# Optimization experiments

Hardware: AMD Instinct MI355X
Metric: run time of the kernel (lower is better)

The kernel has to match this reference:

```python
import jax, jax.numpy as jnp
import numpy as np

IN_MODES = (4, 4, 6, 8)  # prod = 768 = d_model; same modes for input and output
D_MODEL = 768
N_HEADS = 12
D_HEAD = D_MODEL // N_HEADS
SCALE = 1.0 / np.sqrt(D_HEAD)
TT_RANKS = (1, 32, 64, 32, 1)


def tt_linear(x, c0, c1, c2, c3, b):
    # TT-factorized linear: cores c_k have shape (r_{k-1}, m_k, n_k, r_k)
    # with in/out modes IN_MODES. x: [B, S, 768]
    B, S, D = x.shape
    t = x.reshape(B * S, *IN_MODES)                     # n i j k l over in-modes
    t = jnp.einsum('nijkl,mir->njklmr', t, c0[0])       # contract n1, r0=1 squeezed
    t = jnp.einsum('njklmr,rpjs->nklmps', t, c1)        # contract n2 and rank r1
    t = jnp.einsum('nklmps,sqkt->nlmpqt', t, c2)        # contract n3 and rank r2
    t = jnp.einsum('nlmpqt,tul->nmpqu', t, c3[..., 0])  # contract n4 and rank r3, r4=1
    return t.reshape(B, S, D) + b                        # out-modes m,p,q,u -> 768


def _make_tt_params(key):
    ks = jax.random.split(key, 4)
    cores = []
    for i in range(4):
        shape = (TT_RANKS[i], IN_MODES[i], IN_MODES[i], TT_RANKS[i + 1])
        cores.append(jax.random.normal(ks[i], shape, jnp.float32) * 0.05)
    bias = jnp.zeros((D_MODEL,), jnp.float32)
    return cores, bias


def setup_inputs() -> dict:
    key = jax.random.key(0)
    kx, kq, kk, kv, ko = jax.random.split(key, 5)
    B, S = 2, 2048
    x = jax.random.normal(kx, (B, S, D_MODEL), jnp.float32)
    mask = jnp.tril(jnp.ones((S, S), dtype=bool))[None, None]  # causal [1,1,S,S]
    out = {'x': x, 'mask': mask}
    for name, k in (('q', kq), ('k', kk), ('v', kv), ('o', ko)):
        cores, bias = _make_tt_params(k)
        for i in range(4):
            out[f'{name}c{i}'] = cores[i]
        out[f'{name}b'] = bias
    return out


def reference(x, mask,
              qc0, qc1, qc2, qc3, qb,
              kc0, kc1, kc2, kc3, kb,
              vc0, vc1, vc2, vc3, vb,
              oc0, oc1, oc2, oc3, ob):
    B, S, _ = x.shape
    q = tt_linear(x, qc0, qc1, qc2, qc3, qb)
    k = tt_linear(x, kc0, kc1, kc2, kc3, kb)
    v = tt_linear(x, vc0, vc1, vc2, vc3, vb)
    # [B, S, H, Dh] -> [B, H, S, Dh]
    q = q.reshape(B, S, N_HEADS, D_HEAD).transpose(0, 2, 1, 3)
    k = k.reshape(B, S, N_HEADS, D_HEAD).transpose(0, 2, 1, 3)
    v = v.reshape(B, S, N_HEADS, D_HEAD).transpose(0, 2, 1, 3)
    scores = jnp.einsum('bhqd,bhkd->bhqk', q, k) * SCALE  # full O(S^2) scores
    scores = jnp.where(mask, scores, jnp.float32(-10000.0))  # masked_fill(mask==0,-1e4)
    attn = jax.nn.softmax(scores, axis=-1)  # dropout is identity at eval
    out = jnp.einsum('bhqk,bhkd->bhqd', attn, v)
    out = out.transpose(0, 2, 1, 3).reshape(B, S, D_MODEL)
    return tt_linear(out, oc0, oc1, oc2, oc3, ob)
```

## Files before the change

### kernel.cpp

```cpp
#include <hip/hip_runtime.h>
#include <cstddef>
#include <cstdint>

#define D_MODEL 768
#define N_HEADS 12
#define SEQ 2048
#define BATCH 2
#define NROWS (BATCH * SEQ)
#define W_ELEMS (D_MODEL * D_MODEL)
#define Y_ELEMS (NROWS * D_MODEL)

typedef __attribute__((ext_vector_type(8))) short bf16x8;
typedef __attribute__((ext_vector_type(4))) float f32x4;

struct TTPtrs {
    const float* c0[4];
    const float* c1[4];
    const float* c2[4];
    const float* c3[4];
};

__device__ __forceinline__ float bf2f(uint16_t u) {
    union { uint32_t u; float f; } c; c.u = ((uint32_t)u) << 16; return c.f;
}
__device__ __forceinline__ uint16_t f2bf(float f) {
    union { float f; uint32_t u; } c; c.f = f;
    uint32_t x = c.u + 0x7fffu + ((c.u >> 16) & 1u);
    return (uint16_t)(x >> 16);
}
__device__ __forceinline__ uint32_t cvtpk(float lo, float hi) {
    uint32_t r;
    asm("v_cvt_pk_bf16_f32 %0, %1, %2" : "=v"(r) : "v"(lo), "v"(hi));
    return r;
}
__device__ __forceinline__ void glds16(const void* g, void* l) {
    auto gp = reinterpret_cast<const __attribute__((address_space(1))) uint32_t*>(
        reinterpret_cast<uintptr_t>(g));
    auto lp = reinterpret_cast<__attribute__((address_space(3))) uint32_t*>(
        reinterpret_cast<uintptr_t>(l));
    __builtin_amdgcn_global_load_lds(gp, lp, 16, 0, 0);
}

__global__ __launch_bounds__(256) void pre_kernel(TTPtrs P, float* __restrict__ wsA,
                                                  const float* __restrict__ x,
                                                  uint16_t* __restrict__ xb) {
    const int bx = blockIdx.x;
    if (bx < 256) {
        const int mat = bx >> 6;
        const float* c0 = P.c0[mat];
        const float* c1 = P.c1[mat];
        float* A = wsA + mat * 16384;
        int idx = (bx & 63) * 256 + threadIdx.x;
        int s = idx & 63, pj = (idx >> 6) & 15, mi = idx >> 10;
        float acc = 0.f;
        #pragma unroll 8
        for (int r = 0; r < 32; r++)
            acc = fmaf(c0[mi * 32 + r], c1[(r * 16 + pj) * 64 + s], acc);
        A[idx] = acc;
    } else {
        int idx = ((bx - 256) * 256 + threadIdx.x) * 4;
        float4 v = *(const float4*)(x + idx);
        *(uint2*)(xb + idx) = make_uint2(cvtpk(v.x, v.y), cvtpk(v.z, v.w));
    }
}

__global__ __launch_bounds__(256) void tt_buildB(TTPtrs P, const float* __restrict__ wsA,
                                                 float* __restrict__ wsB) {
    const int mat = blockIdx.y;
    const float* c2 = P.c2[mat];
    const float* A = wsA + mat * 16384;
    float* B = wsB + (size_t)mat * 294912;
    int idx = blockIdx.x * 256 + threadIdx.x;
    int t = idx & 31;
    int rest = idx >> 5;
    int qk = rest % 36;
    int rest2 = rest / 36;
    int pj = rest2 & 15, mi = rest2 >> 4;
    const float* Arow = A + (mi * 16 + pj) * 64;
    float acc = 0.f;
    #pragma unroll 8
    for (int s = 0; s < 64; s++)
        acc = fmaf(Arow[s], c2[(s * 36 + qk) * 32 + t], acc);
    B[idx] = acc;
}

__global__ __launch_bounds__(256) void tt_buildC(TTPtrs P, const float* __restrict__ wsB,
                                                 uint16_t* __restrict__ Wbf) {
    __shared__ float b_lds[36 * 33];
    __shared__ float c_lds[32 * 64];
    const int mat = blockIdx.y;
    const int mipj = blockIdx.x;
    const int mi = mipj >> 4, pj = mipj & 15;
    const int m = mi >> 2, i = mi & 3, p = pj >> 2, j = pj & 3;
    const float* Bsrc = wsB + (size_t)mat * 294912 + (size_t)mipj * 1152;
    const float* c3 = P.c3[mat];
    uint16_t* Wt = Wbf + (size_t)mat * W_ELEMS;
    const int tid = threadIdx.x;

    for (int e = tid; e < 1152; e += 256) {
        int qk = e >> 5, t = e & 31;
        b_lds[qk * 33 + t] = Bsrc[e];
    }
    for (int e = tid; e < 2048; e += 256)
        c_lds[e] = c3[e];
    __syncthreads();

    const int outbase = (m * 4 + p) * 48;
    const int inbase = (i * 4 + j) * 48;
    #pragma unroll
    for (int n = 0; n < 9; n++) {
        int idx = n * 256 + tid;
        int qu = idx / 48, kl = idx % 48;
        int q = qu >> 3, u = qu & 7, k = kl >> 3, l = kl & 7;
        const float* brow = &b_lds[(q * 6 + k) * 33];
        const float* crow = &c_lds[u * 8 + l];
        float acc = 0.f;
        #pragma unroll 8
        for (int t = 0; t < 32; t++)
            acc = fmaf(brow[t], crow[t * 64], acc);
        Wt[(size_t)(outbase + qu) * D_MODEL + inbase + kl] = f2bf(acc);
    }
}

template <int MODE>
__global__ __launch_bounds__(256) void gemm_mfma(const uint16_t* __restrict__ X,
                                                 const uint16_t* __restrict__ Wall,
                                                 const float* __restrict__ b0,
                                                 const float* __restrict__ b1,
                                                 const float* __restrict__ b2,
                                                 void* __restrict__ Yall,
                                                 uint16_t* __restrict__ Vt) {
    __shared__ uint16_t lds[2][8192];
    const int z = blockIdx.z;
    const uint16_t* W = Wall + (size_t)z * W_ELEMS;
    const float* bias = (z == 0) ? b0 : (z == 1 ? b1 : b2);
    const int m0 = blockIdx.x * 128, n0 = blockIdx.y * 128;
    const int tid = threadIdx.x, w = tid >> 6, l = tid & 63;
    const int wr = w >> 1, wc = w & 1;
    const int l15 = l & 15, lg = l >> 4;

    const int srow = w * 32 + (l >> 2);
    const int scol = ((l & 3) ^ ((l >> 2) & 3)) * 8;
    const uint16_t* Abase = X + (size_t)(m0 + srow) * D_MODEL + scol;
    const uint16_t* Bbase = W + (size_t)(n0 + srow) * D_MODEL + scol;

    f32x4 acc[4][4];
    #pragma unroll
    for (int mi = 0; mi < 4; ++mi)
        #pragma unroll
        for (int ni = 0; ni < 4; ++ni) acc[mi][ni] = (f32x4){0.f, 0.f, 0.f, 0.f};

    auto stage = [&](int buf, int kt) {
        const uint16_t* A0 = Abase + kt * 32;
        const uint16_t* B0 = Bbase + kt * 32;
        glds16(A0, &lds[buf][w * 1024]);
        glds16(A0 + 16 * D_MODEL, &lds[buf][w * 1024 + 512]);
        glds16(B0, &lds[buf][4096 + w * 1024]);
        glds16(B0 + 16 * D_MODEL, &lds[buf][4096 + w * 1024 + 512]);
    };

    stage(0, 0);
    __syncthreads();
    const int roff = ((lg ^ (l & 3)) << 3);
    for (int kt = 0; kt < 24; ++kt) {
        int cur = kt & 1;
        if (kt < 23) stage(cur ^ 1, kt + 1);
        const uint16_t* As = &lds[cur][0];
        const uint16_t* Bs = &lds[cur][4096];
        bf16x8 a[4], bb[4];
        #pragma unroll
        for (int mi = 0; mi < 4; ++mi)
            a[mi] = *(const bf16x8*)(As + (wr * 64 + mi * 16 + l15) * 32 + roff);
        #pragma unroll
        for (int ni = 0; ni < 4; ++ni)
            bb[ni] = *(const bf16x8*)(Bs + (wc * 64 + ni * 16 + l15) * 32 + roff);
        #pragma unroll
        for (int mi = 0; mi < 4; ++mi)
            #pragma unroll
            for (int ni = 0; ni < 4; ++ni)
                acc[mi][ni] = __builtin_amdgcn_mfma_f32_16x16x32_bf16(
                    a[mi], bb[ni], acc[mi][ni], 0, 0, 0);
        __syncthreads();
    }

    float bv[4];
    #pragma unroll
    for (int ni = 0; ni < 4; ++ni) bv[ni] = bias[n0 + wc * 64 + ni * 16 + l15];

    if (MODE == 1 && z == 2) {
        uint16_t* T = &lds[0][0];
        #pragma unroll
        for (int mi = 0; mi < 4; ++mi) {
            int row = wr * 64 + mi * 16 + lg * 4;
            #pragma unroll
            for (int ni = 0; ni < 4; ++ni) {
                int col = wc * 64 + ni * 16 + l15;
                float v0 = acc[mi][ni][0] + bv[ni], v1 = acc[mi][ni][1] + bv[ni];
                float v2 = acc[mi][ni][2] + bv[ni], v3 = acc[mi][ni][3] + bv[ni];
                int byte = (col << 8) + (row << 1);
                byte ^= (((col & 31) ^ (row >> 6)) << 3);
                *(uint2*)((char*)T + byte) = make_uint2(cvtpk(v0, v1), cvtpk(v2, v3));
            }
        }
        __syncthreads();
        int col = tid >> 1, half = tid & 1;
        int gcol = n0 + col;
        int bb_ = m0 >> 11;
        int s = (m0 & 2047) + half * 64;
        uint16_t* dst = Vt + ((size_t)(bb_ * 12 + (gcol >> 6)) * 64 + (gcol & 63)) * 2048 + s;
        uint2 tv[16];
        #pragma unroll
        for (int k = 0; k < 16; ++k) {
            int r = half * 64 + k * 4;
            int byte = (col << 8) + (r << 1);
            byte ^= (((col & 31) ^ (r >> 6)) << 3);
            tv[k] = *(const uint2*)((const char*)T + byte);
        }
        #pragma unroll
        for (int k = 0; k < 8; ++k)
            *(uint4*)(dst + k * 8) = make_uint4(tv[2 * k].x, tv[2 * k].y,
                                                tv[2 * k + 1].x, tv[2 * k + 1].y);
    } else {
        #pragma unroll
        for (int mi = 0; mi < 4; ++mi)
            #pragma unroll
            for (int ni = 0; ni < 4; ++ni)
                #pragma unroll
                for (int r = 0; r < 4; ++r) {
                    int row = m0 + wr * 64 + mi * 16 + lg * 4 + r;
                    int col = n0 + wc * 64 + ni * 16 + l15;
                    float v = acc[mi][ni][r] + bv[ni];
                    if (MODE == 1)
                        ((uint16_t*)Yall + (size_t)z * Y_ELEMS)[(size_t)row * D_MODEL + col] = f2bf(v);
                    else
                        ((float*)Yall)[(size_t)row * D_MODEL + col] = v;
                }
    }
}

__global__ __launch_bounds__(256) void attn_mfma(const uint16_t* __restrict__ Q,
                                                 const uint16_t* __restrict__ K,
                                                 const uint16_t* __restrict__ Vt,
                                                 uint16_t* __restrict__ pO1,
                                                 uint16_t* __restrict__ pO2,
                                                 float* __restrict__ tbuf) {
    __shared__ uint16_t ks[2][4096];
    __shared__ uint16_t vs[2][4096];
    __shared__ uint16_t ps[4][1024];

    const int bx = blockIdx.x;
    const int u = bx / 24;
    const int bh = bx % 24;
    int g, c;
    if (u < 32)      { g = u >> 2,            c = u & 3; }
    else if (u < 56) { int t = u - 32; g = 8 + t / 3,  c = t % 3; }
    else if (u < 72) { int t = u - 56; g = 16 + (t >> 1), c = t & 1; }
    else             { g = 24 + (u - 72),     c = 0; }
    const int qt = 31 - g;
    const int ktlo = c * 8;
    const int kthi = min(ktlo + 7, qt);
    const int nkt = kthi - ktlo + 1;

    const int b = bh / 12, h = bh % 12;
    const int tid = threadIdx.x, w = tid >> 6, l = tid & 63;
    const int l15 = l & 15, lg = l >> 4;
    const size_t headoff = (size_t)b * SEQ * D_MODEL + h * 64;
    const size_t vhead = ((size_t)(b * 12 + h)) << 17;
    const int sc8 = ((l & 7) ^ ((l >> 3) & 7)) * 8;
    const int srow = w * 16 + (l >> 3);

    const float QS = 0.125f * 1.44269504088896f;
    bf16x8 qf[2];
    {
        const uint16_t* qp = Q + headoff + (size_t)(qt * 64 + w * 16 + l15) * D_MODEL + lg * 8;
        #pragma unroll
        for (int ds = 0; ds < 2; ++ds) {
            bf16x8 qv = *(const bf16x8*)(qp + ds * 32);
            #pragma unroll
            for (int j = 0; j < 8; ++j)
                qf[ds][j] = (short)f2bf(bf2f((uint16_t)qv[j]) * QS);
        }
    }

    float m_ = -3e38f, l_ = 0.f;
    f32x4 oacc[4];
    #pragma unroll
    for (int ni = 0; ni < 4; ++ni) oacc[ni] = (f32x4){0.f, 0.f, 0.f, 0.f};
    const int qglob = qt * 64 + w * 16 + l15;

    auto stage = [&](int buf, int kt) {
        const uint16_t* ksrc = K + headoff + (size_t)(kt * 64 + srow) * D_MODEL + sc8;
        glds16(ksrc, &ks[buf][w * 1024]);
        glds16(ksrc + 8 * D_MODEL, &ks[buf][w * 1024 + 512]);
        const uint16_t* vsrc = Vt + vhead + (size_t)srow * SEQ + kt * 64 + sc8;
        glds16(vsrc, &vs[buf][w * 1024]);
        glds16(vsrc + 8 * SEQ, &vs[buf][w * 1024 + 512]);
    };

    stage(0, ktlo);
    for (int it = 0; it < nkt; ++it) {
        const int kt = ktlo + it;
        const int cur = it & 1;
        __syncthreads();
        if (it + 1 < nkt) stage(cur ^ 1, kt + 1);

        f32x4 sacc[4];
        #pragma unroll
        for (int ki = 0; ki < 4; ++ki) sacc[ki] = (f32x4){0.f, 0.f, 0.f, 0.f};
        __builtin_amdgcn_s_setprio(1);
        #pragma unroll
        for (int ds = 0; ds < 2; ++ds)
            #pragma unroll
            for (int ki = 0; ki < 4; ++ki) {
                int byte = (ki * 16 + l15) * 128 + ((((ds << 2) + lg) ^ (l15 & 7)) << 4);
                bf16x8 ak = *(const bf16x8*)((const char*)&ks[cur][0] + byte);
                sacc[ki] = __builtin_amdgcn_mfma_f32_16x16x32_bf16(ak, qf[ds], sacc[ki], 0, 0, 0);
            }
        __builtin_amdgcn_s_setprio(0);

        const bool diag = (kt == qt);
        float sv[16];
        #pragma unroll
        for (int ki = 0; ki < 4; ++ki)
            #pragma unroll
            for (int r = 0; r < 4; ++r) {
                float s = sacc[ki][r];
                if (diag) {
                    int key = kt * 64 + ki * 16 + lg * 4 + r;
                    if (key > qglob) s = -3e38f;
                }
                sv[ki * 4 + r] = s;
            }
        float mx = fmaxf(fmaxf(sv[0], sv[1]), sv[2]);
        #pragma unroll
        for (int i = 3; i < 15; i += 2) mx = fmaxf(fmaxf(mx, sv[i]), sv[i + 1]);
        mx = fmaxf(mx, sv[15]);
        mx = fmaxf(mx, __shfl_xor(mx, 16));
        mx = fmaxf(mx, __shfl_xor(mx, 32));
        if (__any(mx > m_ + 11.54f)) {
            float mnew = fmaxf(m_, mx);
            float alpha = __builtin_amdgcn_exp2f(m_ - mnew);
            l_ *= alpha;
            float a0 = __shfl(alpha, lg * 4 + 0), a1 = __shfl(alpha, lg * 4 + 1);
            float a2 = __shfl(alpha, lg * 4 + 2), a3 = __shfl(alpha, lg * 4 + 3);
            #pragma unroll
            for (int ni = 0; ni < 4; ++ni) {
                oacc[ni][0] *= a0; oacc[ni][1] *= a1;
                oacc[ni][2] *= a2; oacc[ni][3] *= a3;
            }
            m_ = mnew;
        }
        float sum = 0.f;
        uint32_t pk[8];
        #pragma unroll
        for (int i = 0; i < 16; i += 2) {
            float p0 = __builtin_amdgcn_exp2f(sv[i] - m_);
            float p1 = __builtin_amdgcn_exp2f(sv[i + 1] - m_);
            sum += p0 + p1;
            pk[i >> 1] = cvtpk(p0, p1);
        }
        sum += __shfl_xor(sum, 16);
        sum += __shfl_xor(sum, 32);
        l_ += sum;

        uint16_t* psw = &ps[w][0];
        #pragma unroll
        for (int ki = 0; ki < 4; ++ki) {
            int byte = (l15 * 128 + ki * 32 + lg * 8) ^ ((l15 & 7) << 4);
            *(uint2*)((char*)psw + byte) = make_uint2(pk[ki * 2], pk[ki * 2 + 1]);
        }
        asm volatile("s_waitcnt lgkmcnt(0)" ::: "memory");
        __builtin_amdgcn_sched_barrier(0);

        __builtin_amdgcn_s_setprio(1);
        #pragma unroll
        for (int kss = 0; kss < 2; ++kss) {
            int pbyte = l15 * 128 + ((((kss << 2) + lg) ^ (l15 & 7)) << 4);
            bf16x8 ap = *(const bf16x8*)((const char*)psw + pbyte);
            #pragma unroll
            for (int ni = 0; ni < 4; ++ni) {
                int vbyte = (ni * 16 + l15) * 128 + ((((kss << 2) + lg) ^ (l15 & 7)) << 4);
                bf16x8 bv = *(const bf16x8*)((const char*)&vs[cur][0] + vbyte);
                oacc[ni] = __builtin_amdgcn_mfma_f32_16x16x32_bf16(ap, bv, oacc[ni], 0, 0, 0);
            }
        }
        __builtin_amdgcn_s_setprio(0);
    }

    float li0 = 1.f / __shfl(l_, lg * 4 + 0), li1 = 1.f / __shfl(l_, lg * 4 + 1);
    float li2 = 1.f / __shfl(l_, lg * 4 + 2), li3 = 1.f / __shfl(l_, lg * 4 + 3);
    uint16_t* op = (bx < 1536) ? (pO1 + (size_t)bx * 4096)
                               : (pO2 + (size_t)(bx - 1536) * 4096);
    #pragma unroll
    for (int ni = 0; ni < 4; ++ni) {
        int col = ni * 16 + l15;
        int rbase = (w * 16 + lg * 4) * 64 + col;
        op[rbase + 0 * 64] = f2bf(oacc[ni][0] * li0);
        op[rbase + 1 * 64] = f2bf(oacc[ni][1] * li1);
        op[rbase + 2 * 64] = f2bf(oacc[ni][2] * li2);
        op[rbase + 3 * 64] = f2bf(oacc[ni][3] * li3);
    }
    if (lg == 0)
        tbuf[(size_t)bx * 64 + w * 16 + l15] = m_ + __log2f(l_);
}

__global__ __launch_bounds__(256) void attn_combine(const uint16_t* __restrict__ pO1,
                                                    const uint16_t* __restrict__ pO2,
                                                    const float* __restrict__ tbuf,
                                                    uint16_t* __restrict__ Obf) {
    __shared__ float t_lds[4][64];
    const int bx = blockIdx.x;
    const int qt = bx & 31, bh = bx >> 5;
    const int b = bh / 12, h = bh % 12;
    const int g = 31 - qt;
    const int u_base = (g < 8) ? 4 * g : (g < 16) ? 32 + 3 * (g - 8)
                     : (g < 24) ? 56 + 2 * (g - 16) : 72 + (g - 24);
    const int nc = (g < 8) ? 4 : (g < 16) ? 3 : (g < 24) ? 2 : 1;
    const int tid = threadIdx.x;
    if (tid < nc * 64) {
        int c = tid >> 6, q = tid & 63;
        t_lds[c][q] = tbuf[(size_t)((u_base + c) * 24 + bh) * 64 + q];
    }
    __syncthreads();

    const int q = tid >> 2, d0 = (tid & 3) * 16;
    float tmax = t_lds[0][q];
    for (int c = 1; c < nc; ++c) tmax = fmaxf(tmax, t_lds[c][q]);
    float acc[16];
    #pragma unroll
    for (int j = 0; j < 16; ++j) acc[j] = 0.f;
    float denom = 0.f;
    for (int c = 0; c < nc; ++c) {
        float wgt = __builtin_amdgcn_exp2f(t_lds[c][q] - tmax);
        denom += wgt;
        int ug = (u_base + c) * 24 + bh;
        const uint16_t* op = (ug < 1536) ? (pO1 + (size_t)ug * 4096)
                                         : (pO2 + (size_t)(ug - 1536) * 4096);
        bf16x8 v0 = *(const bf16x8*)(op + q * 64 + d0);
        bf16x8 v1 = *(const bf16x8*)(op + q * 64 + d0 + 8);
        #pragma unroll
        for (int j = 0; j < 8; ++j) {
            acc[j]     += bf2f((uint16_t)v0[j]) * wgt;
            acc[8 + j] += bf2f((uint16_t)v1[j]) * wgt;
        }
    }
    float inv = 1.f / denom;
    uint32_t outp[8];
    #pragma unroll
    for (int j = 0; j < 8; ++j)
        outp[j] = cvtpk(acc[2 * j] * inv, acc[2 * j + 1] * inv);
    size_t rb = (size_t)(b * SEQ + qt * 64 + q) * D_MODEL + h * 64 + d0;
    *(uint4*)(Obf + rb)     = make_uint4(outp[0], outp[1], outp[2], outp[3]);
    *(uint4*)(Obf + rb + 8) = make_uint4(outp[4], outp[5], outp[6], outp[7]);
}

extern "C" void kernel_launch(void* const* d_in, const int* in_sizes, int n_in,
                              void* d_out, int out_size, void* d_ws, size_t ws_size,
                              hipStream_t stream) {
    const float* x = (const float*)d_in[0];
    TTPtrs P;
    const float* biases[4];
    const int base[4] = {2, 7, 12, 17};
    for (int t = 0; t < 4; t++) {
        P.c0[t] = (const float*)d_in[base[t] + 0];
        P.c1[t] = (const float*)d_in[base[t] + 1];
        P.c2[t] = (const float*)d_in[base[t] + 2];
        P.c3[t] = (const float*)d_in[base[t] + 3];
        biases[t] = (const float*)d_in[base[t] + 4];
    }

    char* ws = (char*)d_ws;
    float* wsA = (float*)(ws + 0);
    float* wsB = (float*)(ws + 262144);
    uint16_t* Wbf = (uint16_t*)(ws + 4980736);
    uint16_t* xbf = (uint16_t*)(ws + 9699328);
    uint16_t* pO2 = (uint16_t*)(ws + 9699328);
    float* tbuf = (float*)(ws + 12845056);
    uint16_t* Qbf = (uint16_t*)(ws + 15990784);
    uint16_t* Kbf = (uint16_t*)(ws + 22282240);
    uint16_t* Vtbf = (uint16_t*)(ws + 28573696);
    uint16_t* Obf = (uint16_t*)(ws + 34865152);
    uint16_t* pO1 = (uint16_t*)d_out;
    (void)Kbf;

    pre_kernel<<<dim3(256 + 3072), 256, 0, stream>>>(P, wsA, x, xbf);
    tt_buildB<<<dim3(1152, 4), 256, 0, stream>>>(P, wsA, wsB);
    tt_buildC<<<dim3(256, 4), 256, 0, stream>>>(P, wsB, Wbf);

    gemm_mfma<1><<<dim3(32, 6, 3), 256, 0, stream>>>(xbf, Wbf, biases[0], biases[1],
                                                     biases[2], (void*)Qbf, Vtbf);
    attn_mfma<<<dim3(1920), 256, 0, stream>>>(Qbf, Kbf, Vtbf, pO1, pO2, tbuf);
    attn_combine<<<dim3(768), 256, 0, stream>>>(pO1, pO2, tbuf, Obf);

    gemm_mfma<0><<<dim3(32, 6, 1), 256, 0, stream>>>(Obf, Wbf + 3 * (size_t)W_ELEMS,
                                                     biases[3], biases[3], biases[3],
                                                     d_out, nullptr);
}
```

Measured before the change: 237.8 us.

## Fuse three TT weight-build kernels and x conversion into one kernel

Merges the pre_kernel (A = c0·c1), tt_buildB (B = A·c2) and tt_buildC (W = B·c3) stages into a single wbuild kernel. Each block recomputes its 64-entry A row and its 1152-entry B slice in shared memory instead of writing them to workspace and reading them back. This removes two kernel launches and the global round-trips for the intermediates. In exchange, each block reads c2 from global memory (L2-cached) and does a longer serial stage, so per-block latency grows.

```diff
diff --git a/kernel.cpp b/kernel.cpp
--- a/kernel.cpp
+++ b/kernel.cpp
@@ -41,68 +41,50 @@
     __builtin_amdgcn_global_load_lds(gp, lp, 16, 0, 0);
 }
 
-__global__ __launch_bounds__(256) void pre_kernel(TTPtrs P, float* __restrict__ wsA,
-                                                  const float* __restrict__ x,
-                                                  uint16_t* __restrict__ xb) {
+__global__ __launch_bounds__(256) void wbuild(TTPtrs P, uint16_t* __restrict__ Wbf,
+                                              const float* __restrict__ x,
+                                              uint16_t* __restrict__ xb) {
+    __shared__ float c_lds[2048];
+    __shared__ float a_lds[64];
+    __shared__ float b_lds[36 * 33];
     const int bx = blockIdx.x;
-    if (bx < 256) {
-        const int mat = bx >> 6;
+    const int tid = threadIdx.x;
+    if (bx >= 1024) {
+        int idx = ((bx - 1024) * 256 + tid) * 4;
+        float4 v = *(const float4*)(x + idx);
+        *(uint2*)(xb + idx) = make_uint2(cvtpk(v.x, v.y), cvtpk(v.z, v.w));
+        return;
+    }
+    const int mat = bx >> 8, mipj = bx & 255;
+    const int mi = mipj >> 4, pj = mipj & 15;
+    const int m = mi >> 2, i = mi & 3, p = pj >> 2, j = pj & 3;
+    const float* c2 = P.c2[mat];
+    uint16_t* Wt = Wbf + (size_t)mat * W_ELEMS;
+
+    for (int e = tid; e < 2048; e += 256)
+        c_lds[e] = P.c3[mat][e];
+    if (tid < 64) {
         const float* c0 = P.c0[mat];
         const float* c1 = P.c1[mat];
-        float* A = wsA + mat * 16384;
-        int idx = (bx & 63) * 256 + threadIdx.x;
-        int s = idx & 63, pj = (idx >> 6) & 15, mi = idx >> 10;
         float acc = 0.f;
         #pragma unroll 8
         for (int r = 0; r < 32; r++)
-            acc = fmaf(c0[mi * 32 + r], c1[(r * 16 + pj) * 64 + s], acc);
-        A[idx] = acc;
-    } else {
-        int idx = ((bx - 256) * 256 + threadIdx.x) * 4;
-        float4 v = *(const float4*)(x + idx);
-        *(uint2*)(xb + idx) = make_uint2(cvtpk(v.x, v.y), cvtpk(v.z, v.w));
-    }
-}
-
-__global__ __launch_bounds__(256) void tt_buildB(TTPtrs P, const float* __restrict__ wsA,
-                                                 float* __restrict__ wsB) {
-    const int mat = blockIdx.y;
-    const float* c2 = P.c2[mat];
-    const float* A = wsA + mat * 16384;
-    float* B = wsB + (size_t)mat * 294912;
-    int idx = blockIdx.x * 256 + threadIdx.x;
-    int t = idx & 31;
-    int rest = idx >> 5;
-    int qk = rest % 36;
-    int rest2 = rest / 36;
-    int pj = rest2 & 15, mi = rest2 >> 4;
-    const float* Arow = A + (mi * 16 + pj) * 64;
-    float acc = 0.f;
-    #pragma unroll 8
-    for (int s = 0; s < 64; s++)
-        acc = fmaf(Arow[s], c2[(s * 36 + qk) * 32 + t], acc);
-    B[idx] = acc;
-}
-
-__global__ __launch_bounds__(256) void tt_buildC(TTPtrs P, const float* __restrict__ wsB,
-                                                 uint16_t* __restrict__ Wbf) {
-    __shared__ float b_lds[36 * 33];
-    __shared__ float c_lds[32 * 64];
-    const int mat = blockIdx.y;
-    const int mipj = blockIdx.x;
-    const int mi = mipj >> 4, pj = mipj & 15;
-    const int m = mi >> 2, i = mi & 3, p = pj >> 2, j = pj & 3;
-    const float* Bsrc = wsB + (size_t)mat * 294912 + (size_t)mipj * 1152;
-    const float* c3 = P.c3[mat];
-    uint16_t* Wt = Wbf + (size_t)mat * W_ELEMS;
-    const int tid = threadIdx.x;
-
-    for (int e = tid; e < 1152; e += 256) {
-        int qk = e >> 5, t = e & 31;
-        b_lds[qk * 33 + t] = Bsrc[e];
-    }
-    for (int e = tid; e < 2048; e += 256)
-        c_lds[e] = c3[e];
+            acc = fmaf(c0[mi * 32 + r], c1[(r * 16 + pj) * 64 + tid], acc);
+        a_lds[tid] = acc;
+    }
+    __syncthreads();
+
+    #pragma unroll
+    for (int n = 0; n < 5; ++n) {
+        int idx = n * 256 + tid;
+        if (idx < 1152) {
+            float acc = 0.f;
+            #pragma unroll 8
+            for (int s = 0; s < 64; s++)
+                acc = fmaf(a_lds[s], c2[s * 1152 + idx], acc);
+            b_lds[(idx >> 5) * 33 + (idx & 31)] = acc;
+        }
+    }
     __syncthreads();
 
     const int outbase = (m * 4 + p) * 48;
@@ -470,8 +452,6 @@
     }
 
     char* ws = (char*)d_ws;
-    float* wsA = (float*)(ws + 0);
-    float* wsB = (float*)(ws + 262144);
     uint16_t* Wbf = (uint16_t*)(ws + 4980736);
     uint16_t* xbf = (uint16_t*)(ws + 9699328);
     uint16_t* pO2 = (uint16_t*)(ws + 9699328);
@@ -483,9 +463,7 @@
     uint16_t* pO1 = (uint16_t*)d_out;
     (void)Kbf;
 
-    pre_kernel<<<dim3(256 + 3072), 256, 0, stream>>>(P, wsA, x, xbf);
-    tt_buildB<<<dim3(1152, 4), 256, 0, stream>>>(P, wsA, wsB);
-    tt_buildC<<<dim3(256, 4), 256, 0, stream>>>(P, wsB, Wbf);
+    wbuild<<<dim3(1024 + 3072), 256, 0, stream>>>(P, Wbf, x, xbf);
 
     gemm_mfma<1><<<dim3(32, 6, 3), 256, 0, stream>>>(xbf, Wbf, biases[0], biases[1],
                                                      biases[2], (void*)Qbf, Vtbf);
```

New measurement: 230.0 us. -3.3%, faster.
